# Performance work log

Hardware: AMD Instinct MI355X
Metric: run time of the kernel (lower is better)

The kernel has to match this reference:

```python
import jax, jax.numpy as jnp
import numpy as np

B, S, D = 4, 4096, 1024

def setup_inputs() -> dict:
    key = jax.random.key(0)
    ks = jax.random.split(key, 7)
    s = 1.0 / np.sqrt(D)
    return {
        "x":   jax.random.normal(ks[0], (B, S, D), dtype=jnp.float32),
        "Wq":  jax.random.uniform(ks[1], (D, D), jnp.float32, -s, s),
        "bq":  jax.random.uniform(ks[2], (D,),   jnp.float32, -s, s),
        "Wk":  jax.random.uniform(ks[3], (D, D), jnp.float32, -s, s),
        "bk":  jax.random.uniform(ks[4], (D,),   jnp.float32, -s, s),
        "Wv":  jax.random.uniform(ks[5], (D, D), jnp.float32, -s, s),
        "bv":  jax.random.uniform(ks[6], (D,),   jnp.float32, -s, s),
    }

def reference(x, Wq, bq, Wk, bk, Wv, bv):
    # Linear projections (torch Linear: x @ W.T + b; here W stored as [in, out])
    Q = jnp.einsum('bsd,df->bsf', x, Wq) + bq
    K = jnp.einsum('bsd,df->bsf', x, Wk) + bk
    V = jnp.einsum('bsd,df->bsf', x, Wv) + bv
    scale = 1.0 / jnp.sqrt(jnp.asarray(D, dtype=jnp.float32))
    scores = jnp.einsum('bqd,bkd->bqk', Q, K) * scale  # [B, S, S]
    attn = jax.nn.softmax(scores, axis=-1)
    return jnp.einsum('bqk,bkd->bqd', attn, V)
```

## Files before the change

kernel.cpp:

```cpp
#include <hip/hip_runtime.h>
#include <hip/hip_bf16.h>
#include <stdint.h>


typedef __attribute__((ext_vector_type(8))) short bf16x8;
typedef __attribute__((ext_vector_type(4))) float f32x4;

static __device__ __forceinline__ unsigned short f2b(float f) {
  union { float f; unsigned u; } x; x.f = f;
  unsigned u = x.u;
  u += 0x7fffu + ((u >> 16) & 1u);
  return (unsigned short)(u >> 16);
}
static __device__ __forceinline__ float b2f(unsigned short s) {
  union { unsigned u; float f; } x; x.u = ((unsigned)s) << 16;
  return x.f;
}

static __device__ __forceinline__ void gl_lds16(const void* g, void* l) {
  __builtin_amdgcn_global_load_lds(
      (const __attribute__((address_space(1))) void*)(uintptr_t)(g),
      (__attribute__((address_space(3))) void*)(uint32_t)(uintptr_t)(l),
      16, 0, 0);
}

__global__ void convert_x(const float* __restrict__ in,
                          unsigned short* __restrict__ out, int n8) {
  int i = blockIdx.x * blockDim.x + threadIdx.x;
  if (i >= n8) return;
  const float4* p = (const float4*)in + (size_t)i * 2;
  float4 a = p[0], b = p[1];
  bf16x8 o;
  o[0] = (short)f2b(a.x); o[1] = (short)f2b(a.y);
  o[2] = (short)f2b(a.z); o[3] = (short)f2b(a.w);
  o[4] = (short)f2b(b.x); o[5] = (short)f2b(b.y);
  o[6] = (short)f2b(b.z); o[7] = (short)f2b(b.w);
  ((bf16x8*)out)[i] = o;
}

__global__ void transpose_w(const float* __restrict__ in,
                            unsigned short* __restrict__ out) {
  __shared__ float tile[32][33];
  const int tx = threadIdx.x;
  const int x = blockIdx.x * 32 + tx;
  const int y0 = blockIdx.y * 32;
  for (int j = threadIdx.y; j < 32; j += 8)
    tile[j][tx] = in[(size_t)(y0 + j) * 1024 + x];
  __syncthreads();
  const int ox = blockIdx.y * 32 + tx;
  const int oy0 = blockIdx.x * 32;
  for (int j = threadIdx.y; j < 32; j += 8)
    out[(size_t)(oy0 + j) * 1024 + ox] = f2b(tile[tx][j]);
}

template <int OUTF>
__global__ __launch_bounds__(512, 2)
void gemm256(const unsigned short* __restrict__ A, long lda, long sAz,
             const unsigned short* __restrict__ B, long ldb, long sBz,
             void* __restrict__ Cv, long ldc, long sCz,
             const float* __restrict__ bias, int bias_mode,
             int K, float alpha) {
  __shared__ __align__(16) unsigned short As[2][256 * 64];
  __shared__ __align__(16) unsigned short Bs[2][256 * 64];

  const int t = threadIdx.x;
  const int wid = t >> 6, lane = t & 63;
  const int wm = wid >> 2, wn = wid & 3;
  const int fr = lane & 15, fq = lane >> 4;
  const long bm = (long)blockIdx.y * 256;
  const long bn = (long)blockIdx.x * 256;
  const unsigned short* Ab = A + (size_t)blockIdx.z * sAz;
  const unsigned short* Bb = B + (size_t)blockIdx.z * sBz;

  const int sr = t >> 3;
  const int scol = 8 * ((t & 7) ^ (sr & 7));
  const unsigned short* Ag = Ab + (bm + sr) * lda + scol;
  const unsigned short* Bg = Bb + (bn + sr) * ldb + scol;
  const int ldsw = wid * 512;

  const int NT = K >> 6;
  f32x4 acc[8][4] = {};

#define STAGE(XS, Xg, ld, kt, h, bidx)                                        \
  do {                                                                        \
    gl_lds16(Xg + (size_t)((h) * 128) * (ld) + (size_t)(kt) * 64,             \
             &XS[bidx][(h) * 128 * 64 + ldsw]);                               \
    gl_lds16(Xg + (size_t)((h) * 128 + 64) * (ld) + (size_t)(kt) * 64,        \
             &XS[bidx][((h) * 128 + 64) * 64 + ldsw]);                        \
  } while (0)

  auto rdA = [&](int bidx, int i, int kh) {
    int row = wm * 128 + i * 16 + fr;
    int inb = (kh * 64 + fq * 16) ^ ((fr & 7) << 4);
    return *(const bf16x8*)((const char*)&As[bidx][0] + row * 128 + inb);
  };
  auto rdB = [&](int bidx, int j, int kh) {
    int row = wn * 64 + j * 16 + fr;
    int inb = (kh * 64 + fq * 16) ^ ((fr & 7) << 4);
    return *(const bf16x8*)((const char*)&Bs[bidx][0] + row * 128 + inb);
  };

  STAGE(As, Ag, lda, 0, 0, 0); STAGE(As, Ag, lda, 0, 1, 0);
  STAGE(Bs, Bg, ldb, 0, 0, 0); STAGE(Bs, Bg, ldb, 0, 1, 0);
  STAGE(Bs, Bg, ldb, 1, 0, 1); STAGE(Bs, Bg, ldb, 1, 1, 1);
  asm volatile("s_waitcnt vmcnt(4)" ::: "memory");
  asm volatile("s_barrier" ::: "memory");

  bf16x8 bfr[4][2];
  for (int tt = 0; tt < NT; ++tt) {
    const int bidx = tt & 1;
#pragma unroll
    for (int p = 0; p < 4; ++p) {
      bf16x8 ar[2][2];
      if (p == 0) {
#pragma unroll
        for (int j = 0; j < 4; ++j) {
          bfr[j][0] = rdB(bidx, j, 0);
          bfr[j][1] = rdB(bidx, j, 1);
        }
      }
#pragma unroll
      for (int ii = 0; ii < 2; ++ii) {
        ar[ii][0] = rdA(bidx, p * 2 + ii, 0);
        ar[ii][1] = rdA(bidx, p * 2 + ii, 1);
      }
      if (p == 0 && tt + 1 < NT) STAGE(As, Ag, lda, tt + 1, 0, (tt + 1) & 1);
      if (p == 1 && tt + 1 < NT) STAGE(As, Ag, lda, tt + 1, 1, (tt + 1) & 1);
      if (p == 2 && tt + 2 < NT) STAGE(Bs, Bg, ldb, tt + 2, 0, tt & 1);
      if (p == 3 && tt + 2 < NT) STAGE(Bs, Bg, ldb, tt + 2, 1, tt & 1);
      asm volatile("s_barrier" ::: "memory");
      __builtin_amdgcn_s_setprio(1);
#pragma unroll
      for (int ii = 0; ii < 2; ++ii)
#pragma unroll
        for (int j = 0; j < 4; ++j) {
          acc[p * 2 + ii][j] = __builtin_amdgcn_mfma_f32_16x16x32_bf16(
              ar[ii][0], bfr[j][0], acc[p * 2 + ii][j], 0, 0, 0);
          acc[p * 2 + ii][j] = __builtin_amdgcn_mfma_f32_16x16x32_bf16(
              ar[ii][1], bfr[j][1], acc[p * 2 + ii][j], 0, 0, 0);
        }
      __builtin_amdgcn_s_setprio(0);
      if (p == 3) {
        if (tt + 2 < NT)
          asm volatile("s_waitcnt vmcnt(4)" ::: "memory");
        else if (tt + 1 < NT)
          asm volatile("s_waitcnt vmcnt(0)" ::: "memory");
      }
      asm volatile("s_barrier" ::: "memory");
    }
  }
#undef STAGE

  char* Cb = (char*)Cv + (size_t)blockIdx.z * sCz * (OUTF ? 4 : 2);
  const long crow0 = bm + wm * 128 + fq * 4;
  const long ccol0 = bn + wn * 64 + fr;
#pragma unroll
  for (int i = 0; i < 8; ++i) {
#pragma unroll
    for (int j = 0; j < 4; ++j) {
      const long col = ccol0 + j * 16;
      float badd_c = (bias_mode == 1) ? bias[col] : 0.0f;
#pragma unroll
      for (int r = 0; r < 4; ++r) {
        const long row = crow0 + i * 16 + r;
        float v = acc[i][j][r] * alpha + badd_c;
        if (bias_mode == 2) v += bias[row];
        if (OUTF)
          ((float*)Cb)[row * ldc + col] = v;
        else
          ((unsigned short*)Cb)[row * ldc + col] = f2b(v);
      }
    }
  }
}

__global__ __launch_bounds__(256)
void softmax_rows(unsigned short* __restrict__ S) {
  const int t = threadIdx.x;
  unsigned short* row = S + (size_t)blockIdx.x * 4096;
  const bf16x8* p = (const bf16x8*)row;
  bf16x8 u0 = p[t * 2], u1 = p[t * 2 + 1];

  float v[16];
  float m = -1e30f;
#pragma unroll
  for (int j = 0; j < 8; j++) { v[j] = b2f((unsigned short)u0[j]); }
#pragma unroll
  for (int j = 0; j < 8; j++) { v[8 + j] = b2f((unsigned short)u1[j]); }
#pragma unroll
  for (int j = 0; j < 16; j++) m = fmaxf(m, v[j]);

#pragma unroll
  for (int off = 32; off > 0; off >>= 1) m = fmaxf(m, __shfl_xor(m, off));
  __shared__ float redm[4];
  if ((t & 63) == 0) redm[t >> 6] = m;
  __syncthreads();
  m = fmaxf(fmaxf(redm[0], redm[1]), fmaxf(redm[2], redm[3]));

  float s = 0.0f;
#pragma unroll
  for (int j = 0; j < 16; j++) { v[j] = __expf(v[j] - m); s += v[j]; }
#pragma unroll
  for (int off = 32; off > 0; off >>= 1) s += __shfl_xor(s, off);
  __shared__ float reds[4];
  if ((t & 63) == 0) reds[t >> 6] = s;
  __syncthreads();
  s = reds[0] + reds[1] + reds[2] + reds[3];
  const float inv = 1.0f / s;

  bf16x8 o0, o1;
#pragma unroll
  for (int j = 0; j < 8; j++) o0[j] = (short)f2b(v[j] * inv);
#pragma unroll
  for (int j = 0; j < 8; j++) o1[j] = (short)f2b(v[8 + j] * inv);
  bf16x8* q = (bf16x8*)row;
  q[t * 2] = o0;
  q[t * 2 + 1] = o1;
}

extern "C" void kernel_launch(void* const* d_in, const int* in_sizes, int n_in,
                              void* d_out, int out_size, void* d_ws,
                              size_t ws_size, hipStream_t stream) {
  const float* x  = (const float*)d_in[0];
  const float* Wq = (const float*)d_in[1];
  const float* bq = (const float*)d_in[2];
  const float* Wk = (const float*)d_in[3];
  const float* bk = (const float*)d_in[4];
  const float* Wv = (const float*)d_in[5];
  const float* bv = (const float*)d_in[6];
  float* out = (float*)d_out;

  const int Bb = 4, S = 4096, D = 1024;
  const long BS = (long)Bb * S;
  const size_t MiB = 1u << 20;

  char* base = (char*)d_ws;
  unsigned short* Wqt = (unsigned short*)(base);
  unsigned short* Wkt = (unsigned short*)(base + 2 * MiB);
  unsigned short* Wvt = (unsigned short*)(base + 4 * MiB);
  unsigned short* Qb  = (unsigned short*)(base + 6 * MiB);
  unsigned short* Kb  = (unsigned short*)(base + 38 * MiB);
  unsigned short* Vt  = (unsigned short*)(base + 70 * MiB);
  unsigned short* xb  = (unsigned short*)(base + 102 * MiB);
  unsigned short* Sb  = xb;
  const bool batched = ws_size >= (size_t)(102 + 128) * MiB;

  const int n8 = (int)(BS * D / 8);
  convert_x<<<n8 / 256, 256, 0, stream>>>(x, xb, n8);

  dim3 tb(32, 8), tg(32, 32);
  transpose_w<<<tg, tb, 0, stream>>>(Wq, Wqt);
  transpose_w<<<tg, tb, 0, stream>>>(Wk, Wkt);
  transpose_w<<<tg, tb, 0, stream>>>(Wv, Wvt);

  gemm256<0><<<dim3(D / 256, BS / 256, 1), 512, 0, stream>>>(
      xb, D, 0, Wqt, D, 0, Qb, D, 0, bq, 1, D, 1.0f);
  gemm256<0><<<dim3(D / 256, BS / 256, 1), 512, 0, stream>>>(
      xb, D, 0, Wkt, D, 0, Kb, D, 0, bk, 1, D, 1.0f);
  gemm256<0><<<dim3(BS / 256, D / 256, 1), 512, 0, stream>>>(
      Wvt, D, 0, xb, D, 0, Vt, BS, 0, bv, 2, D, 1.0f);

  const float scale = 0.03125f;
  if (batched) {
    gemm256<0><<<dim3(S / 256, S / 256, Bb), 512, 0, stream>>>(
        Qb, D, (long)S * D, Kb, D, (long)S * D, Sb, S, (long)S * S,
        nullptr, 0, D, scale);
    softmax_rows<<<Bb * S, 256, 0, stream>>>(Sb);
    gemm256<1><<<dim3(D / 256, S / 256, Bb), 512, 0, stream>>>(
        Sb, S, (long)S * S, Vt, BS, (long)S, out, D, (long)S * D,
        nullptr, 0, S, 1.0f);
  } else {
    for (int b = 0; b < Bb; b++) {
      const unsigned short* Qp = Qb + (long)b * S * D;
      const unsigned short* Kp = Kb + (long)b * S * D;
      gemm256<0><<<dim3(S / 256, S / 256, 1), 512, 0, stream>>>(
          Qp, D, 0, Kp, D, 0, Sb, S, 0, nullptr, 0, D, scale);
      softmax_rows<<<S, 256, 0, stream>>>(Sb);
      gemm256<1><<<dim3(D / 256, S / 256, 1), 512, 0, stream>>>(
          Sb, S, 0, Vt + (long)b * S, BS, 0, out + (long)b * S * D, D, 0,
          nullptr, 0, S, 1.0f);
    }
  }
}
```

Measured before the change: 483.3 us.

## Replace per-phase barriers with one barrier per k-tile and register double-buffered A fragments

The GEMM main loop drops the staggered per-phase staging and its two barriers per phase. It now issues all next-tile A and B loads at the start of each k-tile and synchronises once with vmcnt(0) and a barrier at the end of the tile. A fragments are prefetched one phase ahead into a second register set, so LDS reads overlap the MFMAs. This cuts barrier count and tries to hide LDS latency, at the cost of prefetch depth for B (one tile instead of two), a full vmcnt(0) wait every tile, and more VGPRs.

After: 468.8 us. -3.0%, faster.

```diff
diff --git a/kernel.cpp b/kernel.cpp
--- a/kernel.cpp
+++ b/kernel.cpp
@@ -102,34 +102,40 @@
 
   STAGE(As, Ag, lda, 0, 0, 0); STAGE(As, Ag, lda, 0, 1, 0);
   STAGE(Bs, Bg, ldb, 0, 0, 0); STAGE(Bs, Bg, ldb, 0, 1, 0);
-  STAGE(Bs, Bg, ldb, 1, 0, 1); STAGE(Bs, Bg, ldb, 1, 1, 1);
-  asm volatile("s_waitcnt vmcnt(4)" ::: "memory");
+  asm volatile("s_waitcnt vmcnt(0)" ::: "memory");
   asm volatile("s_barrier" ::: "memory");
 
-  bf16x8 bfr[4][2];
   for (int tt = 0; tt < NT; ++tt) {
     const int bidx = tt & 1;
+    const int nb = (tt + 1) & 1;
+    bf16x8 bfr[4][2], ar[2][2], arn[2][2];
+
+#pragma unroll
+    for (int j = 0; j < 4; ++j) {
+      bfr[j][0] = rdB(bidx, j, 0);
+      bfr[j][1] = rdB(bidx, j, 1);
+    }
+#pragma unroll
+    for (int ii = 0; ii < 2; ++ii) {
+      ar[ii][0] = rdA(bidx, ii, 0);
+      ar[ii][1] = rdA(bidx, ii, 1);
+    }
+
+    if (tt + 1 < NT) {
+      STAGE(As, Ag, lda, tt + 1, 0, nb); STAGE(As, Ag, lda, tt + 1, 1, nb);
+      STAGE(Bs, Bg, ldb, tt + 1, 0, nb); STAGE(Bs, Bg, ldb, tt + 1, 1, nb);
+    }
+
+    __builtin_amdgcn_s_setprio(1);
 #pragma unroll
     for (int p = 0; p < 4; ++p) {
-      bf16x8 ar[2][2];
-      if (p == 0) {
-#pragma unroll
-        for (int j = 0; j < 4; ++j) {
-          bfr[j][0] = rdB(bidx, j, 0);
-          bfr[j][1] = rdB(bidx, j, 1);
+      if (p < 3) {
+#pragma unroll
+        for (int ii = 0; ii < 2; ++ii) {
+          arn[ii][0] = rdA(bidx, (p + 1) * 2 + ii, 0);
+          arn[ii][1] = rdA(bidx, (p + 1) * 2 + ii, 1);
         }
       }
-#pragma unroll
-      for (int ii = 0; ii < 2; ++ii) {
-        ar[ii][0] = rdA(bidx, p * 2 + ii, 0);
-        ar[ii][1] = rdA(bidx, p * 2 + ii, 1);
-      }
-      if (p == 0 && tt + 1 < NT) STAGE(As, Ag, lda, tt + 1, 0, (tt + 1) & 1);
-      if (p == 1 && tt + 1 < NT) STAGE(As, Ag, lda, tt + 1, 1, (tt + 1) & 1);
-      if (p == 2 && tt + 2 < NT) STAGE(Bs, Bg, ldb, tt + 2, 0, tt & 1);
-      if (p == 3 && tt + 2 < NT) STAGE(Bs, Bg, ldb, tt + 2, 1, tt & 1);
-      asm volatile("s_barrier" ::: "memory");
-      __builtin_amdgcn_s_setprio(1);
 #pragma unroll
       for (int ii = 0; ii < 2; ++ii)
 #pragma unroll
@@ -139,15 +145,18 @@
           acc[p * 2 + ii][j] = __builtin_amdgcn_mfma_f32_16x16x32_bf16(
               ar[ii][1], bfr[j][1], acc[p * 2 + ii][j], 0, 0, 0);
         }
-      __builtin_amdgcn_s_setprio(0);
-      if (p == 3) {
-        if (tt + 2 < NT)
-          asm volatile("s_waitcnt vmcnt(4)" ::: "memory");
-        else if (tt + 1 < NT)
-          asm volatile("s_waitcnt vmcnt(0)" ::: "memory");
+      if (p < 3) {
+#pragma unroll
+        for (int ii = 0; ii < 2; ++ii) {
+          ar[ii][0] = arn[ii][0];
+          ar[ii][1] = arn[ii][1];
+        }
       }
-      asm volatile("s_barrier" ::: "memory");
-    }
+    }
+    __builtin_amdgcn_s_setprio(0);
+
+    asm volatile("s_waitcnt vmcnt(0)" ::: "memory");
+    asm volatile("s_barrier" ::: "memory");
   }
 #undef STAGE
 
```
